# Kernel optimization log

Hardware: AMD Instinct MI355X
Metric: run time of the kernel (lower is better)

Reference implementation:

```python
import jax, jax.numpy as jnp
import numpy as np

NINP, NHID, NTOK, NLAYERS, BSZ = 4096, 512, 50257, 2, 32
T_ENC, T_DEC = 80, 40


def lstm_layer(x, h0, c0, Wih, Whh, b):
    """Single LSTM layer over a [T,B,in] sequence; PyTorch gate order i,f,g,o."""
    def step(carry, xt):
        h, c = carry
        z = xt @ Wih.T + h @ Whh.T + b  # [B, 4H]
        i, f, g, o = jnp.split(z, 4, axis=-1)
        c = jax.nn.sigmoid(f) * c + jax.nn.sigmoid(i) * jnp.tanh(g)
        h = jax.nn.sigmoid(o) * jnp.tanh(c)
        return (h, c), h
    (hN, cN), ys = jax.lax.scan(step, (h0, c0), x)
    return ys, hN, cN


def multi_lstm(x, h0, c0, params):
    """Stacked LSTM; params = list of (Wih, Whh, b) per layer."""
    hs, cs = [], []
    y = x
    for l, (Wih, Whh, b) in enumerate(params):
        y, hN, cN = lstm_layer(y, h0[l], c0[l], Wih, Whh, b)
        hs.append(hN); cs.append(cN)
    return y, jnp.stack(hs), jnp.stack(cs)


def setup_inputs():
    key = jax.random.key(0)
    ks = iter(jax.random.split(key, 32))
    def rn(shape, scale=0.05):
        return (jax.random.normal(next(ks), shape, dtype=jnp.float32) * scale)
    H4 = 4 * NHID
    d = {}
    d["inp"] = rn((T_ENC, BSZ, NINP), 1.0)
    for name in ("hid1_h", "hid1_c", "hid2_h", "hid2_c"):
        d[name] = jnp.zeros((NLAYERS, BSZ, NHID), jnp.float32)
    # lstm1: layer0 in=NINP, layer1 in=NHID (b = b_ih + b_hh fused)
    d["l1_Wih0"] = rn((H4, NINP)); d["l1_Whh0"] = rn((H4, NHID)); d["l1_b0"] = rn((H4,))
    d["l1_Wih1"] = rn((H4, NHID)); d["l1_Whh1"] = rn((H4, NHID)); d["l1_b1"] = rn((H4,))
    # lstm2: layer0 in=2*NHID, layer1 in=NHID
    d["l2_Wih0"] = rn((H4, 2 * NHID)); d["l2_Whh0"] = rn((H4, NHID)); d["l2_b0"] = rn((H4,))
    d["l2_Wih1"] = rn((H4, NHID)); d["l2_Whh1"] = rn((H4, NHID)); d["l2_b1"] = rn((H4,))
    d["W_out"] = rn((NTOK, NHID)); d["b_out"] = rn((NTOK,))
    d["W_emb"] = rn((NHID, NTOK)); d["b_emb"] = rn((NHID,))
    d["target_len"] = T_DEC
    return d


def reference(inp, hid1_h, hid1_c, hid2_h, hid2_c,
              l1_Wih0, l1_Whh0, l1_b0, l1_Wih1, l1_Whh1, l1_b1,
              l2_Wih0, l2_Whh0, l2_b0, l2_Wih1, l2_Whh1, l2_b1,
              W_out, b_out, W_emb, b_emb, target_len):
    p1 = [(l1_Wih0, l1_Whh0, l1_b0), (l1_Wih1, l1_Whh1, l1_b1)]
    p2 = [(l2_Wih0, l2_Whh0, l2_b0), (l2_Wih1, l2_Whh1, l2_b1)]
    T, B, ninp = inp.shape
    H = hid1_h.shape[-1]
    # --- encoding stage ---
    out1, h1, c1 = multi_lstm(inp, hid1_h, hid1_c, p1)
    pad_h = jnp.zeros((T, B, H), inp.dtype)
    _, h2, c2 = multi_lstm(jnp.concatenate([pad_h, out1], axis=-1), hid2_h, hid2_c, p2)
    # --- decoding stage ---
    pad_in = jnp.zeros((target_len, B, ninp), inp.dtype)
    out1d, _, _ = multi_lstm(pad_in, h1, c1, p1)
    # vocab2emb(one-hot BOS at index 0) = W_emb[:, 0] + b_emb; never updated in
    # the original loop (variable-name bug), so it is constant over decode steps,
    # making the per-step loop equivalent to one lstm2 scan.
    bos_emb = W_emb[:, 0] + b_emb  # [H]
    bos = jnp.broadcast_to(bos_emb, (target_len, B, H))
    out2d, _, _ = multi_lstm(jnp.concatenate([bos, out1d], axis=-1), h2, c2, p2)
    logits = jnp.einsum('tbh,vh->tbv', out2d, W_out) + b_out  # [T_dec, B, V]
    return jax.nn.log_softmax(logits, axis=-1)
```

## Files before the change

kernel.cpp:

```cpp
#include <hip/hip_runtime.h>
#include <hip/hip_bf16.h>
#include <cstddef>

#define NINP 4096
#define NHID 512
#define G4   2048
#define NTOK 50257
#define BSZ  32
#define T_ENC 80
#define T_DEC 40
#define DQ   4

typedef __attribute__((ext_vector_type(4))) float  f32x4;
typedef __attribute__((ext_vector_type(4))) __bf16 bf16x4;
typedef __attribute__((ext_vector_type(8))) __bf16 bf16x8;

__device__ __forceinline__ int sw_off(int r, int k) {
    return r * 128 + ((((k >> 3) ^ (r & 7)) << 4) | ((k & 7) << 1));
}
__device__ __forceinline__ int swA(int r, int k) {
    return r * 256 + ((((k >> 3) ^ (r & 7)) << 4) | ((k & 7) << 1));
}
__device__ __forceinline__ int sw512(int r, int k) {
    return r * 1024 + ((((k >> 3) ^ (r & 7)) << 4) | ((k & 7) << 1));
}

__device__ __forceinline__ void split4(const float4& v, bf16x4& h, bf16x4& l) {
    float a0 = v.x, a1 = v.y, a2 = v.z, a3 = v.w;
    __bf16 h0 = (__bf16)a0, h1 = (__bf16)a1, h2 = (__bf16)a2, h3 = (__bf16)a3;
    h[0] = h0; h[1] = h1; h[2] = h2; h[3] = h3;
    l[0] = (__bf16)(a0 - (float)h0);
    l[1] = (__bf16)(a1 - (float)h1);
    l[2] = (__bf16)(a2 - (float)h2);
    l[3] = (__bf16)(a3 - (float)h3);
}

__device__ __forceinline__ bf16x4 hi4(const float4& v) {
    bf16x4 h; h[0] = (__bf16)v.x; h[1] = (__bf16)v.y;
    h[2] = (__bf16)v.z; h[3] = (__bf16)v.w; return h;
}

__device__ __forceinline__ void split8(const float4& a, const float4& b,
                                       bf16x8& h, bf16x8& l) {
    float x[8] = {a.x, a.y, a.z, a.w, b.x, b.y, b.z, b.w};
    #pragma unroll
    for (int i = 0; i < 8; i++) {
        __bf16 hb = (__bf16)x[i];
        h[i] = hb; l[i] = (__bf16)(x[i] - (float)hb);
    }
}

__device__ __forceinline__ bf16x8 to_bf16x8(const float4& a, const float4& b) {
    bf16x8 r;
    r[0]=(__bf16)a.x; r[1]=(__bf16)a.y; r[2]=(__bf16)a.z; r[3]=(__bf16)a.w;
    r[4]=(__bf16)b.x; r[5]=(__bf16)b.y; r[6]=(__bf16)b.z; r[7]=(__bf16)b.w;
    return r;
}

__device__ __forceinline__ void unpack8(const uint4& a, const uint4& b,
                                        bf16x8& h, bf16x8& l) {
    unsigned u[8] = {a.x, a.y, a.z, a.w, b.x, b.y, b.z, b.w};
    union { unsigned short s; __bf16 v; } t;
    #pragma unroll
    for (int i = 0; i < 8; i++) {
        t.s = (unsigned short)(u[i] & 0xffff); h[i] = t.v;
        t.s = (unsigned short)(u[i] >> 16);    l[i] = t.v;
    }
}
__device__ __forceinline__ bf16x8 unpack_hi8(const uint4& a, const uint4& b) {
    unsigned u[8] = {a.x, a.y, a.z, a.w, b.x, b.y, b.z, b.w};
    union { unsigned short s; __bf16 v; } t;
    bf16x8 h;
    #pragma unroll
    for (int i = 0; i < 8; i++) { t.s = (unsigned short)(u[i] & 0xffff); h[i] = t.v; }
    return h;
}

__device__ __forceinline__ unsigned pack_hilo(float x) {
    __bf16 hb = (__bf16)x;
    float hf = (float)hb;
    __bf16 lb = (__bf16)(x - hf);
    union { __bf16 b; unsigned short s; } ch, cl;
    ch.b = hb; cl.b = lb;
    return (unsigned)ch.s | ((unsigned)cl.s << 16);
}

__device__ __forceinline__ float fast_sigmoid(float x) {
    return 1.f / (1.f + __expf(-x));
}
__device__ __forceinline__ float fast_tanh(float x) {
    return 1.f - 2.f / (__expf(2.f * x) + 1.f);
}

__global__ __launch_bounds__(256) void gemm_hilo(
    const float* __restrict__ A, int lda,
    const float* __restrict__ B, int ldb,
    const float* __restrict__ bias,
    float* __restrict__ Z, int ldz,
    int N, int K)
{
    __shared__ __align__(16) char lds[49152];
    const int tid  = threadIdx.x;
    const int bm   = blockIdx.y * 128;
    const int bn   = blockIdx.x * 128;
    const int wave = tid >> 6;
    const int lane = tid & 63;
    const int wm   = (wave >> 1) * 64;
    const int wn   = (wave & 1) * 64;
    const int lr   = lane & 15;
    const int kg   = lane >> 4;

    const int rr = tid >> 4;
    const int kk = (tid & 15) * 4;

    f32x4 acc[4][4] = {};

    for (int k0 = 0; k0 < K; k0 += 64) {
        float4 av[8], bv[8];
        #pragma unroll
        for (int i = 0; i < 8; i++) {
            int r = i * 16 + rr;
            av[i] = *(const float4*)&A[(size_t)(bm + r) * lda + k0 + kk];
            int rb = bn + r;
            if (rb < N)
                bv[i] = *(const float4*)&B[(size_t)rb * ldb + k0 + kk];
            else
                bv[i] = make_float4(0.f, 0.f, 0.f, 0.f);
        }
        __syncthreads();
        #pragma unroll
        for (int i = 0; i < 8; i++) {
            int r = i * 16 + rr;
            int off = sw_off(r, kk);
            bf16x4 h, l;
            split4(av[i], h, l);
            *(bf16x4*)(lds + off)         = h;
            *(bf16x4*)(lds + 16384 + off) = l;
            *(bf16x4*)(lds + 32768 + off) = hi4(bv[i]);
        }
        __syncthreads();
        #pragma unroll
        for (int ks = 0; ks < 2; ks++) {
            bf16x8 ah[4], al[4], bh[4];
            const int kbase = ks * 32 + kg * 8;
            #pragma unroll
            for (int f = 0; f < 4; f++) {
                int offA = sw_off(wm + f * 16 + lr, kbase);
                ah[f] = *(const bf16x8*)(lds + offA);
                al[f] = *(const bf16x8*)(lds + 16384 + offA);
                int offB = sw_off(wn + f * 16 + lr, kbase);
                bh[f] = *(const bf16x8*)(lds + 32768 + offB);
            }
            #pragma unroll
            for (int fm = 0; fm < 4; fm++)
                #pragma unroll
                for (int fn = 0; fn < 4; fn++) {
                    acc[fm][fn] = __builtin_amdgcn_mfma_f32_16x16x32_bf16(
                        ah[fm], bh[fn], acc[fm][fn], 0, 0, 0);
                    acc[fm][fn] = __builtin_amdgcn_mfma_f32_16x16x32_bf16(
                        al[fm], bh[fn], acc[fm][fn], 0, 0, 0);
                }
        }
    }

    #pragma unroll
    for (int fn = 0; fn < 4; fn++) {
        int col = bn + wn + fn * 16 + lr;
        if (col < N) {
            float bb = bias ? bias[col] : 0.f;
            #pragma unroll
            for (int fm = 0; fm < 4; fm++) {
                #pragma unroll
                for (int j = 0; j < 4; j++) {
                    int row = bm + wm + fm * 16 + kg * 4 + j;
                    Z[(size_t)row * ldz + col] = acc[fm][fn][j] + bb;
                }
            }
        }
    }
}

__global__ __launch_bounds__(256, 1) void gemm_vocab(
    const __bf16* __restrict__ Ah,
    const float* __restrict__ B,
    const float* __restrict__ bias,
    float* __restrict__ Z)
{
    __shared__ __align__(16) char lds[163840];
    char* ldsB = lds;
    char* ldsA = lds + 131072;

    const int tid  = threadIdx.x;
    const int bn   = blockIdx.x * 128;
    const int wave = tid >> 6;
    const int lane = tid & 63;
    const int wm   = (wave >> 1) * 64;
    const int wn   = (wave & 1) * 64;
    const int lr   = lane & 15;
    const int kg   = lane >> 4;

    #pragma unroll 4
    for (int jj = 0; jj < 32; jj++) {
        int e = tid + jj * 256;
        int row = e >> 6;
        int k = (e & 63) * 8;
        int gr = bn + row;
        float4 v0, v1;
        if (gr < NTOK) {
            v0 = *(const float4*)&B[(size_t)gr * 512 + k];
            v1 = *(const float4*)&B[(size_t)gr * 512 + k + 4];
        } else {
            v0 = make_float4(0.f,0.f,0.f,0.f); v1 = v0;
        }
        *(bf16x8*)(ldsB + sw512(row, k)) = to_bf16x8(v0, v1);
    }

    float bb[4];
    #pragma unroll
    for (int fn = 0; fn < 4; fn++) {
        int col = bn + wn + fn * 16 + lr;
        bb[fn] = (col < NTOK) ? bias[col] : 0.f;
    }
    __syncthreads();

    for (int mt = 0; mt < 10; mt++) {
        f32x4 acc[4][4] = {};
        for (int k0 = 0; k0 < 4; k0++) {
            __syncthreads();
            #pragma unroll
            for (int jj = 0; jj < 8; jj++) {
                int e = tid + jj * 256;
                int row = e >> 4;
                int k = (e & 15) * 8;
                uint4 v = *(const uint4*)&Ah[(size_t)(mt * 128 + row) * 512 + k0 * 128 + k];
                *(uint4*)(ldsA + swA(row, k)) = v;
            }
            __syncthreads();
            #pragma unroll
            for (int ks = 0; ks < 4; ks++) {
                bf16x8 ah[4], bh[4];
                const int ka = ks * 32 + kg * 8;
                #pragma unroll
                for (int f = 0; f < 4; f++) {
                    ah[f] = *(const bf16x8*)(ldsA + swA(wm + f * 16 + lr, ka));
                    bh[f] = *(const bf16x8*)(ldsB + sw512(wn + f * 16 + lr, k0 * 128 + ka));
                }
                #pragma unroll
                for (int fm = 0; fm < 4; fm++)
                    #pragma unroll
                    for (int fn = 0; fn < 4; fn++)
                        acc[fm][fn] = __builtin_amdgcn_mfma_f32_16x16x32_bf16(
                            ah[fm], bh[fn], acc[fm][fn], 0, 0, 0);
            }
        }
        #pragma unroll
        for (int fn = 0; fn < 4; fn++) {
            int col = bn + wn + fn * 16 + lr;
            if (col < NTOK) {
                #pragma unroll
                for (int fm = 0; fm < 4; fm++) {
                    #pragma unroll
                    for (int j = 0; j < 4; j++) {
                        int row = mt * 128 + wm + fm * 16 + kg * 4 + j;
                        Z[(size_t)row * NTOK + col] = acc[fm][fn][j] + bb[fn];
                    }
                }
            }
        }
    }
}

__global__ __launch_bounds__(256, 1) void fused_scan(
    const float* __restrict__ Zx,
    const float* __restrict__ Whh_0, const float* __restrict__ bias_0,
    const float* __restrict__ Wih_1, const float* __restrict__ Whh_1,
    const float* __restrict__ bias_1,
    const float* __restrict__ Wih_2, const float* __restrict__ Whh_2,
    const float* __restrict__ bias_2e, const float* __restrict__ bias_2d,
    const float* __restrict__ Wih_3, const float* __restrict__ Whh_3,
    const float* __restrict__ bias_3,
    const float* __restrict__ hid1_h, const float* __restrict__ hid1_c,
    const float* __restrict__ hid2_h, const float* __restrict__ hid2_c,
    __bf16* __restrict__ dec3h,
    unsigned* hbuf,
    unsigned* flags,
    unsigned* genv)
{
    __shared__ __align__(16) char lds[163840];

    const int tid  = threadIdx.x;
    const int L    = blockIdx.x >> 6;
    const int bidc = blockIdx.x & 63;
    const int wave = tid >> 6;
    const int lane = tid & 63;
    const int mh   = wave >> 1;
    const int ng   = wave & 1;
    const int lr   = lane & 15;
    const int kg   = lane >> 4;
    const int lr3  = lr & 3;
    const int jcbase = bidc * 8;
    const int bq = tid >> 3;
    const int aq = tid & 7;

    const float* Whh = (L==0)?Whh_0:(L==1)?Whh_1:(L==2)?Whh_2:Whh_3;
    const float* Wih = (L==1)?Wih_1:(L==2)?Wih_2:(L==3)?Wih_3:nullptr;
    const int ld_ih  = (L==2)?1024:512;
    const float* be  = (L==0)?bias_0:(L==1)?bias_1:(L==2)?bias_2e:bias_3;
    const float* bd  = (L==2)?bias_2d:be;
    const float* h0  = ((L<2)?hid1_h:hid2_h) + (L&1)*16384;
    const float* c0  = ((L<2)?hid1_c:hid2_c) + (L&1)*16384;
    unsigned* myb       = hbuf + (size_t)L*DQ*16384;
    const unsigned* xsb = hbuf + (size_t)(L>0 ? (L-1) : 0)*DQ*16384;

    {
        int wrow = (bq & 3) * 512 + jcbase + (bq >> 2);
        const float* wr = Whh + (size_t)wrow * 512;
        #pragma unroll
        for (int jj = 0; jj < 8; jj++) {
            int k = aq * 8 + jj * 64;
            *(bf16x8*)(lds + 98304 + sw512(bq, k)) =
                to_bf16x8(*(const float4*)(wr + k), *(const float4*)(wr + k + 4));
        }
        if (Wih) {
            const float* wr2 = Wih + (size_t)wrow * ld_ih;
            #pragma unroll
            for (int jj = 0; jj < 8; jj++) {
                int k = aq * 8 + jj * 64;
                *(bf16x8*)(lds + 131072 + sw512(bq, k)) =
                    to_bf16x8(*(const float4*)(wr2 + k), *(const float4*)(wr2 + k + 4));
            }
        }
    }

    const int hcol = jcbase + ng*4 + (lr >> 2);
    const int grow = lr3 * 512 + hcol;
    const float bbe = be[grow];
    const float bbd = bd[grow];

    float cc[4];
    #pragma unroll
    for (int j = 0; j < 4; j++)
        cc[j] = c0[(mh*16 + kg*4 + j)*512 + hcol];

    const int rowA = mh*16 + lr;
    const int rowB = ng*16 + lr;

    for (int t = 0; t < 120; ++t) {
        if (tid == 0) {
            if (L > 0)
                while (__hip_atomic_load(&genv[L-1], __ATOMIC_RELAXED,
                                         __HIP_MEMORY_SCOPE_AGENT) < (unsigned)(t+1))
                    __builtin_amdgcn_s_sleep(1);
            if (L < 3 && t >= DQ)
                while (__hip_atomic_load(&genv[L+1], __ATOMIC_RELAXED,
                                         __HIP_MEMORY_SCOPE_AGENT) < (unsigned)(t-3))
                    __builtin_amdgcn_s_sleep(1);
            __builtin_amdgcn_fence(__ATOMIC_ACQUIRE, "agent");
        }
        __syncthreads();

        float zx[4] = {0.f, 0.f, 0.f, 0.f};
        if (L == 0 && t < 80) {
            #pragma unroll
            for (int j = 0; j < 4; j++)
                zx[j] = Zx[(size_t)t*(BSZ*G4) + (mh*16+kg*4+j)*G4 + grow];
        }

        if (t == 0) {
            const float* hr = h0 + bq*512;
            #pragma unroll
            for (int jj = 0; jj < 8; jj++) {
                int k = aq*8 + jj*64;
                bf16x8 H, Lo;
                split8(*(const float4*)(hr+k), *(const float4*)(hr+k+4), H, Lo);
                int off = sw512(bq, k);
                *(bf16x8*)(lds + off)         = H;
                *(bf16x8*)(lds + 32768 + off) = Lo;
            }
        } else {
            const unsigned* hs = myb + (size_t)((t-1) & (DQ-1))*16384 + bq*512;
            #pragma unroll
            for (int jj = 0; jj < 8; jj++) {
                int k = aq*8 + jj*64;
                bf16x8 H, Lo;
                unpack8(*(const uint4*)(hs+k), *(const uint4*)(hs+k+4), H, Lo);
                int off = sw512(bq, k);
                *(bf16x8*)(lds + off)         = H;
                *(bf16x8*)(lds + 32768 + off) = Lo;
            }
        }
        if (L > 0) {
            const unsigned* xp = xsb + (size_t)(t & (DQ-1))*16384 + bq*512;
            #pragma unroll
            for (int jj = 0; jj < 8; jj++) {
                int k = aq*8 + jj*64;
                *(bf16x8*)(lds + 65536 + sw512(bq, k)) =
                    unpack_hi8(*(const uint4*)(xp+k), *(const uint4*)(xp+k+4));
            }
        }
        __syncthreads();

        f32x4 accA = {0.f,0.f,0.f,0.f}, accB = {0.f,0.f,0.f,0.f};
        #pragma unroll
        for (int ks = 0; ks < 16; ++ks) {
            int k = ks*32 + kg*8;
            int offA = sw512(rowA, k);
            bf16x8 ah = *(const bf16x8*)(lds + offA);
            bf16x8 al = *(const bf16x8*)(lds + 32768 + offA);
            bf16x8 bh = *(const bf16x8*)(lds + 98304 + sw512(rowB, k));
            accA = __builtin_amdgcn_mfma_f32_16x16x32_bf16(ah, bh, accA, 0,0,0);
            accB = __builtin_amdgcn_mfma_f32_16x16x32_bf16(al, bh, accB, 0,0,0);
        }
        if (L > 0) {
            #pragma unroll
            for (int ks = 0; ks < 16; ++ks) {
                int k = ks*32 + kg*8;
                bf16x8 ax = *(const bf16x8*)(lds + 65536 + sw512(rowA, k));
                bf16x8 bi = *(const bf16x8*)(lds + 131072 + sw512(rowB, k));
                accA = __builtin_amdgcn_mfma_f32_16x16x32_bf16(ax, bi, accA, 0,0,0);
            }
        }

        const float bbv = (L == 2 && t >= 80) ? bbd : bbe;
        float z[4], t0[4];
        #pragma unroll
        for (int j = 0; j < 4; j++) {
            z[j] = accA[j] + accB[j] + bbv + zx[j];
            t0[j] = (lr3 == 2) ? fast_tanh(z[j]) : fast_sigmoid(z[j]);
        }
        float av[4], cn[4], tc[4], hn[4];
        #pragma unroll
        for (int j = 0; j < 4; j++) {
            float x2 = __shfl_xor(t0[j], 2);
            av[j] = t0[j] * x2;
        }
        #pragma unroll
        for (int j = 0; j < 4; j++) {
            float x1 = __shfl_xor(av[j], 1);
            cn[j] = t0[j] * cc[j] + x1;
            cc[j] = cn[j];
            tc[j] = fast_tanh(cn[j]);
        }
        #pragma unroll
        for (int j = 0; j < 4; j++) {
            float x2b = __shfl_xor(tc[j], 2);
            hn[j] = t0[j] * x2b;
        }

        if (lr3 == 3) {
            unsigned* wb = myb + (size_t)(t & (DQ-1))*16384;
            #pragma unroll
            for (int j = 0; j < 4; j++) {
                int b = mh*16 + kg*4 + j;
                float v = hn[j];
                if (L == 3 && t >= 80)
                    dec3h[(size_t)(t-80)*(BSZ*NHID) + b*512 + hcol] = (__bf16)v;
                __hip_atomic_store(&wb[b*512 + hcol], pack_hilo(v),
                                   __ATOMIC_RELAXED, __HIP_MEMORY_SCOPE_AGENT);
            }
        }

        const unsigned target = (unsigned)(t + 1);
        __syncthreads();
        if (tid == 0) {
            __builtin_amdgcn_fence(__ATOMIC_RELEASE, "agent");
            __hip_atomic_store(&flags[L*64 + bidc], target, __ATOMIC_RELAXED,
                               __HIP_MEMORY_SCOPE_AGENT);
        }
        if (bidc == 0) {
            if (tid < 64) {
                while (__hip_atomic_load(&flags[L*64 + tid], __ATOMIC_RELAXED,
                                         __HIP_MEMORY_SCOPE_AGENT) < target)
                    __builtin_amdgcn_s_sleep(1);
            }
            __syncthreads();
            if (tid == 0)
                __hip_atomic_store(&genv[L], target, __ATOMIC_RELAXED,
                                   __HIP_MEMORY_SCOPE_AGENT);
        }
        if (tid == 0) {
            while (__hip_atomic_load(&genv[L], __ATOMIC_RELAXED,
                                     __HIP_MEMORY_SCOPE_AGENT) < target)
                __builtin_amdgcn_s_sleep(1);
            __builtin_amdgcn_fence(__ATOMIC_ACQUIRE, "agent");
        }
        __syncthreads();
    }
}

__global__ __launch_bounds__(256) void bias2_kernel(
    const float* __restrict__ W_emb,
    const float* __restrict__ b_emb,
    const float* __restrict__ Wih0,
    const float* __restrict__ b0,
    float* __restrict__ bias2)
{
    __shared__ float bos[NHID];
    const int tid = threadIdx.x;
    for (int i = tid; i < NHID; i += 256)
        bos[i] = W_emb[(size_t)i * NTOK] + b_emb[i];
    __syncthreads();
    int j = blockIdx.x * 256 + tid;
    float acc = b0[j];
    for (int k = 0; k < NHID; k++)
        acc += bos[k] * Wih0[(size_t)j * 1024 + k];
    bias2[j] = acc;
}

__global__ __launch_bounds__(256) void logsoftmax_kernel(float* __restrict__ logits)
{
    const size_t row = blockIdx.x;
    float* p = logits + row * (size_t)NTOK;
    const int tid = threadIdx.x;

    float m = -1e30f, s = 0.f;
    for (int i = tid; i < NTOK; i += 256) {
        float x = p[i];
        float mn = fmaxf(m, x);
        s = s * __expf(m - mn) + __expf(x - mn);
        m = mn;
    }
    #pragma unroll
    for (int off = 32; off > 0; off >>= 1) {
        float mo = __shfl_down(m, off);
        float so = __shfl_down(s, off);
        float mn = fmaxf(m, mo);
        s = s * __expf(m - mn) + so * __expf(mo - mn);
        m = mn;
    }
    __shared__ float sm[4], ss[4];
    if ((tid & 63) == 0) { sm[tid >> 6] = m; ss[tid >> 6] = s; }
    __syncthreads();
    float M4 = fmaxf(fmaxf(sm[0], sm[1]), fmaxf(sm[2], sm[3]));
    float S  = ss[0] * __expf(sm[0] - M4) + ss[1] * __expf(sm[1] - M4)
             + ss[2] * __expf(sm[2] - M4) + ss[3] * __expf(sm[3] - M4);
    float lse = M4 + logf(S);
    for (int i = tid; i < NTOK; i += 256) p[i] = p[i] - lse;
}

extern "C" void kernel_launch(void* const* d_in, const int* in_sizes, int n_in,
                              void* d_out, int out_size, void* d_ws, size_t ws_size,
                              hipStream_t stream)
{
    const float* inp     = (const float*)d_in[0];
    const float* hid1_h  = (const float*)d_in[1];
    const float* hid1_c  = (const float*)d_in[2];
    const float* hid2_h  = (const float*)d_in[3];
    const float* hid2_c  = (const float*)d_in[4];
    const float* l1_Wih0 = (const float*)d_in[5];
    const float* l1_Whh0 = (const float*)d_in[6];
    const float* l1_b0   = (const float*)d_in[7];
    const float* l1_Wih1 = (const float*)d_in[8];
    const float* l1_Whh1 = (const float*)d_in[9];
    const float* l1_b1   = (const float*)d_in[10];
    const float* l2_Wih0 = (const float*)d_in[11];
    const float* l2_Whh0 = (const float*)d_in[12];
    const float* l2_b0   = (const float*)d_in[13];
    const float* l2_Wih1 = (const float*)d_in[14];
    const float* l2_Whh1 = (const float*)d_in[15];
    const float* l2_b1   = (const float*)d_in[16];
    const float* W_out   = (const float*)d_in[17];
    const float* b_out   = (const float*)d_in[18];
    const float* W_emb   = (const float*)d_in[19];
    const float* b_emb   = (const float*)d_in[20];

    float* out = (float*)d_out;
    float* ws  = (float*)d_ws;

    float* Zx    = ws;
    float* bias2 = ws + 5242880;
    __bf16* dec3h = (__bf16*)(ws + 5244928);
    unsigned* hbuf  = (unsigned*)(ws + 5572608);
    unsigned* flags = (unsigned*)(ws + 5834752);
    unsigned* genv  = flags + 256;

    (void)hipMemsetAsync(flags, 0, 1040, stream);

    {
        dim3 grid((G4 + 127) / 128, (T_ENC * BSZ) / 128);
        gemm_hilo<<<grid, dim3(256), 0, stream>>>(
            inp, NINP, l1_Wih0, NINP, nullptr, Zx, G4, G4, NINP);
    }
    bias2_kernel<<<8, 256, 0, stream>>>(W_emb, b_emb, l2_Wih0, l2_b0, bias2);

    fused_scan<<<256, 256, 0, stream>>>(
        Zx,
        l1_Whh0, l1_b0,
        l1_Wih1, l1_Whh1, l1_b1,
        l2_Wih0 + 512, l2_Whh0, l2_b0, bias2,
        l2_Wih1, l2_Whh1, l2_b1,
        hid1_h, hid1_c, hid2_h, hid2_c,
        dec3h, hbuf, flags, genv);

    gemm_vocab<<<(NTOK + 127) / 128, dim3(256), 0, stream>>>(
        dec3h, W_out, b_out, out);
    logsoftmax_kernel<<<1280, dim3(256), 0, stream>>>(out);
}
```

Measured before the change: 1.999 ms.

## Replace two-level flag barrier with per-layer atomic counters and tighter wavefront window

The per-step grid synchronisation, where each block writes a flag and block 0 gathers the flags and publishes a generation value, is replaced by one atomic counter per layer that every block increments. Each block then waits only on its own layer's counter plus its neighbouring layers' counters before the next step. This removes a serial aggregation hop and the extra end-of-step spin and barrier. The inter-layer hbuf ring depth (DQ) drops from 4 to 2, reducing buffering slack, so a layer can run at most one step ahead of the layer below it. Many blocks contending on the same counter address and the tighter window can add stalls.

Result: slower. 2.061 ms (+3.1%).

```diff
diff --git a/kernel.cpp b/kernel.cpp
--- a/kernel.cpp
+++ b/kernel.cpp
@@ -9,7 +9,7 @@
 #define BSZ  32
 #define T_ENC 80
 #define T_DEC 40
-#define DQ   4
+#define DQ   2
 
 typedef __attribute__((ext_vector_type(4))) float  f32x4;
 typedef __attribute__((ext_vector_type(4))) __bf16 bf16x4;
@@ -283,8 +283,7 @@
     const float* __restrict__ hid2_h, const float* __restrict__ hid2_c,
     __bf16* __restrict__ dec3h,
     unsigned* hbuf,
-    unsigned* flags,
-    unsigned* genv)
+    unsigned* cnt)
 {
     __shared__ __align__(16) char lds[163840];
 
@@ -347,14 +346,21 @@
 
     for (int t = 0; t < 120; ++t) {
         if (tid == 0) {
-            if (L > 0)
-                while (__hip_atomic_load(&genv[L-1], __ATOMIC_RELAXED,
-                                         __HIP_MEMORY_SCOPE_AGENT) < (unsigned)(t+1))
-                    __builtin_amdgcn_s_sleep(1);
-            if (L < 3 && t >= DQ)
-                while (__hip_atomic_load(&genv[L+1], __ATOMIC_RELAXED,
-                                         __HIP_MEMORY_SCOPE_AGENT) < (unsigned)(t-3))
-                    __builtin_amdgcn_s_sleep(1);
+            const unsigned own = 64u * (unsigned)t;
+            const unsigned up  = 64u * (unsigned)(t + 1);
+            const unsigned dn  = (t >= 1) ? 64u * (unsigned)(t - 1) : 0u;
+            for (;;) {
+                bool ok = __hip_atomic_load(&cnt[L*32], __ATOMIC_RELAXED,
+                                            __HIP_MEMORY_SCOPE_AGENT) >= own;
+                if (L > 0)
+                    ok &= __hip_atomic_load(&cnt[(L-1)*32], __ATOMIC_RELAXED,
+                                            __HIP_MEMORY_SCOPE_AGENT) >= up;
+                if (L < 3)
+                    ok &= __hip_atomic_load(&cnt[(L+1)*32], __ATOMIC_RELAXED,
+                                            __HIP_MEMORY_SCOPE_AGENT) >= dn;
+                if (ok) break;
+                __builtin_amdgcn_s_sleep(1);
+            }
             __builtin_amdgcn_fence(__ATOMIC_ACQUIRE, "agent");
         }
         __syncthreads();
@@ -460,31 +466,12 @@
             }
         }
 
-        const unsigned target = (unsigned)(t + 1);
         __syncthreads();
         if (tid == 0) {
             __builtin_amdgcn_fence(__ATOMIC_RELEASE, "agent");
-            __hip_atomic_store(&flags[L*64 + bidc], target, __ATOMIC_RELAXED,
-                               __HIP_MEMORY_SCOPE_AGENT);
-        }
-        if (bidc == 0) {
-            if (tid < 64) {
-                while (__hip_atomic_load(&flags[L*64 + tid], __ATOMIC_RELAXED,
-                                         __HIP_MEMORY_SCOPE_AGENT) < target)
-                    __builtin_amdgcn_s_sleep(1);
-            }
-            __syncthreads();
-            if (tid == 0)
-                __hip_atomic_store(&genv[L], target, __ATOMIC_RELAXED,
+            __hip_atomic_fetch_add(&cnt[L*32], 1u, __ATOMIC_RELAXED,
                                    __HIP_MEMORY_SCOPE_AGENT);
         }
-        if (tid == 0) {
-            while (__hip_atomic_load(&genv[L], __ATOMIC_RELAXED,
-                                     __HIP_MEMORY_SCOPE_AGENT) < target)
-                __builtin_amdgcn_s_sleep(1);
-            __builtin_amdgcn_fence(__ATOMIC_ACQUIRE, "agent");
-        }
-        __syncthreads();
     }
 }
 
@@ -570,11 +557,10 @@
     float* Zx    = ws;
     float* bias2 = ws + 5242880;
     __bf16* dec3h = (__bf16*)(ws + 5244928);
-    unsigned* hbuf  = (unsigned*)(ws + 5572608);
-    unsigned* flags = (unsigned*)(ws + 5834752);
-    unsigned* genv  = flags + 256;
-
-    (void)hipMemsetAsync(flags, 0, 1040, stream);
+    unsigned* hbuf = (unsigned*)(ws + 5572608);
+    unsigned* cnt  = (unsigned*)(ws + 5703680);
+
+    (void)hipMemsetAsync(cnt, 0, 512, stream);
 
     {
         dim3 grid((G4 + 127) / 128, (T_ENC * BSZ) / 128);
@@ -590,7 +576,7 @@
         l2_Wih0 + 512, l2_Whh0, l2_b0, bias2,
         l2_Wih1, l2_Whh1, l2_b1,
         hid1_h, hid1_c, hid2_h, hid2_c,
-        dec3h, hbuf, flags, genv);
+        dec3h, hbuf, cnt);
 
     gemm_vocab<<<(NTOK + 127) / 128, dim3(256), 0, stream>>>(
         dec3h, W_out, b_out, out);
```
